# Kernel optimization log

Hardware: AMD Instinct MI355X
Metric: run time of the kernel (lower is better)

Reference implementation:

```python
import jax, jax.numpy as jnp
import numpy as np
from jax import lax

B, T, D = 512, 512, 8   # batch, history_steps, input_size
H = 256                  # hidden_size


def setup_inputs() -> dict:
    key = jax.random.key(0)
    k1, k2, k3, k4, k5 = jax.random.split(key, 5)
    history = jax.random.normal(k1, (B, T, D), dtype=jnp.float32)
    s = 1.0 / np.sqrt(H)  # torch default init scale for RNN cells / Linear
    W_ih = jax.random.uniform(k2, (4 * H, D), minval=-s, maxval=s, dtype=jnp.float32)
    W_hh = jax.random.uniform(k3, (4 * H, H), minval=-s, maxval=s, dtype=jnp.float32)
    W_out = jax.random.uniform(k4, (2, H), minval=-s, maxval=s, dtype=jnp.float32)
    b_out = jax.random.uniform(k5, (2,), minval=-s, maxval=s, dtype=jnp.float32)
    return {"history": history, "W_ih": W_ih, "W_hh": W_hh, "W_out": W_out, "b_out": b_out}


def reference(history, W_ih, W_hh, W_out, b_out):
    # LSTMCell unrolled over time (bias=False), with per-step Linear(H,2) head.
    Bs = history.shape[0]
    h0 = jnp.zeros((Bs, H), dtype=history.dtype)
    c0 = jnp.zeros((Bs, H), dtype=history.dtype)

    def step(carry, x_t):
        h, c = carry
        gates = x_t @ W_ih.T + h @ W_hh.T            # [B, 4H]
        i, f, g, o = jnp.split(gates, 4, axis=-1)
        i = jax.nn.sigmoid(i)
        f = jax.nn.sigmoid(f)
        g = jnp.tanh(g)
        o = jax.nn.sigmoid(o)
        c_new = f * c + i * g
        h_new = o * jnp.tanh(c_new)
        logit = h_new @ W_out.T + b_out              # [B, 2]
        return (h_new, c_new), logit

    x_seq = jnp.transpose(history, (1, 0, 2))        # [T, B, D]
    (h_T, c_T), logits = lax.scan(step, (h0, c0), x_seq)
    logits = jnp.transpose(logits, (1, 0, 2))        # [B, T, 2]
    return logits, h_T, c_T
```

## Files before the change

### kernel.cpp

```cpp
#include <hip/hip_runtime.h>


#define T_STEPS 512
#define B_ROWS  512
#define D_IN    8
#define HID     256

typedef _Float16 half2_t __attribute__((ext_vector_type(2)));

#if defined(__has_builtin)
#  if __has_builtin(__builtin_amdgcn_fdot2)
#    define HAVE_FDOT2 1
#  endif
#endif
#ifndef HAVE_FDOT2
#  define HAVE_FDOT2 0
#endif

#define PW2_ENTRIES (128 * HID)
#define PWIH_FLOATS (4 * HID * D_IN)
#define WS_BYTES_NEEDED ((size_t)PW2_ENTRIES * 16 + (size_t)PWIH_FLOATS * 4)

__global__ void prep_kernel(const float* __restrict__ Wih,
                            const float* __restrict__ Whh,
                            uint4* __restrict__ PW2,
                            float* __restrict__ PWih) {
  int p = blockIdx.x * 256 + threadIdx.x;
  if (p < PW2_ENTRIES) {
    int u = p & (HID - 1), k2 = p >> 8;
    unsigned int g[4];
    #pragma unroll
    for (int gi = 0; gi < 4; ++gi) {
      float lo = Whh[(gi * HID + u) * HID + 2 * k2];
      float hi = Whh[(gi * HID + u) * HID + 2 * k2 + 1];
      half2_t hv;
      hv[0] = (_Float16)lo;
      hv[1] = (_Float16)hi;
      g[gi] = __builtin_bit_cast(unsigned int, hv);
    }
    PW2[p] = make_uint4(g[0], g[1], g[2], g[3]);
  } else {
    int q = p - PW2_ENTRIES;
    if (q < PWIH_FLOATS) {
      int gg = q & 3, u = (q >> 2) & (HID - 1), d = q >> 10;
      PWih[q] = Wih[(gg * HID + u) * D_IN + d];
    }
  }
}

__device__ __forceinline__ float sigmoidf_(float x) {
  return 1.f / (1.f + expf(-x));
}
__device__ __forceinline__ float tanhf_(float x) {
  float e = expf(2.f * x);
  return 1.f - 2.f / (e + 1.f);
}

__device__ __forceinline__ float dot2f(unsigned int wbits, unsigned int hbits, float acc) {
  half2_t w = __builtin_bit_cast(half2_t, wbits);
  half2_t h = __builtin_bit_cast(half2_t, hbits);
#if HAVE_FDOT2
  return __builtin_amdgcn_fdot2(w, h, acc, false);
#else
  acc = fmaf((float)w[0], (float)h[0], acc);
  return fmaf((float)w[1], (float)h[1], acc);
#endif
}

template <bool DIRECT>
__global__ __launch_bounds__(1024, 4)
void lstm_kernel(const float* __restrict__ hist,
                 const float* __restrict__ Wih,
                 const float* __restrict__ Whh,
                 const float* __restrict__ Wout,
                 const float* __restrict__ bout,
                 const uint4* __restrict__ PW2,
                 const float4* __restrict__ PWih,
                 float* __restrict__ out) {
  __shared__ float4   h4[HID];
  __shared__ _Float16 h16[HID / 2][4][2];
  __shared__ float    wo[2 * HID];
  __shared__ float    part[4][4][4][HID];

  const int t = threadIdx.x;
  const int u = t & (HID - 1);
  const int q = t >> 8;

  if (t < 2 * HID) wo[t] = Wout[t];
  if (t < HID) h4[t] = make_float4(0.f, 0.f, 0.f, 0.f);
  ((_Float16*)h16)[t] = (_Float16)0.f;
  float c_reg = 0.f, h_reg = 0.f;
  const float b0 = bout[0], b1 = bout[1];
  __syncthreads();

  const int row0 = blockIdx.x * 4;
  const float4* __restrict__ xp0 = (const float4*)(hist + (long)(row0 + 0) * T_STEPS * D_IN);
  const float4* __restrict__ xp1 = (const float4*)(hist + (long)(row0 + 1) * T_STEPS * D_IN);
  const float4* __restrict__ xp2 = (const float4*)(hist + (long)(row0 + 2) * T_STEPS * D_IN);
  const float4* __restrict__ xp3 = (const float4*)(hist + (long)(row0 + 3) * T_STEPS * D_IN);
  const uint4* __restrict__ pwq = DIRECT ? nullptr : (PW2 + (size_t)(32 * q) * HID + u);
  const uint4* __restrict__ h16q = (const uint4*)h16;

  for (int step = 0; step < T_STEPS; ++step) {
    float ai0 = 0.f, ai1 = 0.f, ai2 = 0.f, ai3 = 0.f;
    float af0 = 0.f, af1 = 0.f, af2 = 0.f, af3 = 0.f;
    float ag0 = 0.f, ag1 = 0.f, ag2 = 0.f, ag3 = 0.f;
    float ao0 = 0.f, ao1 = 0.f, ao2 = 0.f, ao3 = 0.f;

    if (q == 0) {
      float4 a0 = xp0[2 * step], bb0 = xp0[2 * step + 1];
      float4 a1 = xp1[2 * step], bb1 = xp1[2 * step + 1];
      float4 a2 = xp2[2 * step], bb2 = xp2[2 * step + 1];
      float4 a3 = xp3[2 * step], bb3 = xp3[2 * step + 1];
      float x0[D_IN] = {a0.x, a0.y, a0.z, a0.w, bb0.x, bb0.y, bb0.z, bb0.w};
      float x1[D_IN] = {a1.x, a1.y, a1.z, a1.w, bb1.x, bb1.y, bb1.z, bb1.w};
      float x2[D_IN] = {a2.x, a2.y, a2.z, a2.w, bb2.x, bb2.y, bb2.z, bb2.w};
      float x3[D_IN] = {a3.x, a3.y, a3.z, a3.w, bb3.x, bb3.y, bb3.z, bb3.w};
      #pragma unroll
      for (int d = 0; d < D_IN; ++d) {
        float4 w;
        if (DIRECT) {
          w.x = Wih[(0 * HID + u) * D_IN + d];
          w.y = Wih[(1 * HID + u) * D_IN + d];
          w.z = Wih[(2 * HID + u) * D_IN + d];
          w.w = Wih[(3 * HID + u) * D_IN + d];
        } else {
          w = PWih[d * HID + u];
        }
        ai0 = fmaf(w.x, x0[d], ai0); af0 = fmaf(w.y, x0[d], af0);
        ag0 = fmaf(w.z, x0[d], ag0); ao0 = fmaf(w.w, x0[d], ao0);
        ai1 = fmaf(w.x, x1[d], ai1); af1 = fmaf(w.y, x1[d], af1);
        ag1 = fmaf(w.z, x1[d], ag1); ao1 = fmaf(w.w, x1[d], ao1);
        ai2 = fmaf(w.x, x2[d], ai2); af2 = fmaf(w.y, x2[d], af2);
        ag2 = fmaf(w.z, x2[d], ag2); ao2 = fmaf(w.w, x2[d], ao2);
        ai3 = fmaf(w.x, x3[d], ai3); af3 = fmaf(w.y, x3[d], af3);
        ag3 = fmaf(w.z, x3[d], ag3); ao3 = fmaf(w.w, x3[d], ao3);
      }
    }

    if (DIRECT) {
      #pragma unroll 8
      for (int kk = 0; kk < 32; ++kk) {
        int k = 2 * (32 * q + kk);
        float wiA = Whh[(0 * HID + u) * HID + k], wiB = Whh[(0 * HID + u) * HID + k + 1];
        float wfA = Whh[(1 * HID + u) * HID + k], wfB = Whh[(1 * HID + u) * HID + k + 1];
        float wgA = Whh[(2 * HID + u) * HID + k], wgB = Whh[(2 * HID + u) * HID + k + 1];
        float woA = Whh[(3 * HID + u) * HID + k], woB = Whh[(3 * HID + u) * HID + k + 1];
        float4 hA = h4[k];
        float4 hB = h4[k + 1];
        ai0 = fmaf(wiA, hA.x, ai0); ai1 = fmaf(wiA, hA.y, ai1);
        ai2 = fmaf(wiA, hA.z, ai2); ai3 = fmaf(wiA, hA.w, ai3);
        ai0 = fmaf(wiB, hB.x, ai0); ai1 = fmaf(wiB, hB.y, ai1);
        ai2 = fmaf(wiB, hB.z, ai2); ai3 = fmaf(wiB, hB.w, ai3);
        af0 = fmaf(wfA, hA.x, af0); af1 = fmaf(wfA, hA.y, af1);
        af2 = fmaf(wfA, hA.z, af2); af3 = fmaf(wfA, hA.w, af3);
        af0 = fmaf(wfB, hB.x, af0); af1 = fmaf(wfB, hB.y, af1);
        af2 = fmaf(wfB, hB.z, af2); af3 = fmaf(wfB, hB.w, af3);
        ag0 = fmaf(wgA, hA.x, ag0); ag1 = fmaf(wgA, hA.y, ag1);
        ag2 = fmaf(wgA, hA.z, ag2); ag3 = fmaf(wgA, hA.w, ag3);
        ag0 = fmaf(wgB, hB.x, ag0); ag1 = fmaf(wgB, hB.y, ag1);
        ag2 = fmaf(wgB, hB.z, ag2); ag3 = fmaf(wgB, hB.w, ag3);
        ao0 = fmaf(woA, hA.x, ao0); ao1 = fmaf(woA, hA.y, ao1);
        ao2 = fmaf(woA, hA.z, ao2); ao3 = fmaf(woA, hA.w, ao3);
        ao0 = fmaf(woB, hB.x, ao0); ao1 = fmaf(woB, hB.y, ao1);
        ao2 = fmaf(woB, hB.z, ao2); ao3 = fmaf(woB, hB.w, ao3);
      }
    } else {
      #pragma unroll 8
      for (int kk = 0; kk < 32; ++kk) {
        uint4 w  = pwq[(size_t)kk * HID];
        uint4 hp = h16q[32 * q + kk];
        ai0 = dot2f(w.x, hp.x, ai0); ai1 = dot2f(w.x, hp.y, ai1);
        ai2 = dot2f(w.x, hp.z, ai2); ai3 = dot2f(w.x, hp.w, ai3);
        af0 = dot2f(w.y, hp.x, af0); af1 = dot2f(w.y, hp.y, af1);
        af2 = dot2f(w.y, hp.z, af2); af3 = dot2f(w.y, hp.w, af3);
        ag0 = dot2f(w.z, hp.x, ag0); ag1 = dot2f(w.z, hp.y, ag1);
        ag2 = dot2f(w.z, hp.z, ag2); ag3 = dot2f(w.z, hp.w, ag3);
        ao0 = dot2f(w.w, hp.x, ao0); ao1 = dot2f(w.w, hp.y, ao1);
        ao2 = dot2f(w.w, hp.z, ao2); ao3 = dot2f(w.w, hp.w, ao3);
      }
    }

    part[q][0][0][u] = ai0; part[q][0][1][u] = ai1; part[q][0][2][u] = ai2; part[q][0][3][u] = ai3;
    part[q][1][0][u] = af0; part[q][1][1][u] = af1; part[q][1][2][u] = af2; part[q][1][3][u] = af3;
    part[q][2][0][u] = ag0; part[q][2][1][u] = ag1; part[q][2][2][u] = ag2; part[q][2][3][u] = ag3;
    part[q][3][0][u] = ao0; part[q][3][1][u] = ao1; part[q][3][2][u] = ao2; part[q][3][3][u] = ao3;

    __syncthreads();

    {
      float gi = part[0][0][q][u] + part[1][0][q][u] + part[2][0][q][u] + part[3][0][q][u];
      float gf = part[0][1][q][u] + part[1][1][q][u] + part[2][1][q][u] + part[3][1][q][u];
      float gg = part[0][2][q][u] + part[1][2][q][u] + part[2][2][q][u] + part[3][2][q][u];
      float go = part[0][3][q][u] + part[1][3][q][u] + part[2][3][q][u] + part[3][3][q][u];
      float iv = sigmoidf_(gi), fv = sigmoidf_(gf);
      float gv = tanhf_(gg),    ov = sigmoidf_(go);
      c_reg = fmaf(fv, c_reg, iv * gv);
      h_reg = ov * tanhf_(c_reg);
      ((float*)h4)[u * 4 + q] = h_reg;
      h16[u >> 1][q][u & 1] = (_Float16)h_reg;
    }

    __syncthreads();

    {
      const int wv = t >> 6;
      if (wv < 8) {
        const int lane = t & 63;
        const int r  = wv >> 1;
        const int lg = wv & 1;
        float partial = 0.f;
        #pragma unroll
        for (int m = 0; m < 4; ++m) {
          int k = lane + 64 * m;
          float4 hv = h4[k];
          float hval = (r == 0) ? hv.x : (r == 1) ? hv.y : (r == 2) ? hv.z : hv.w;
          partial = fmaf(hval, wo[lg * HID + k], partial);
        }
        #pragma unroll
        for (int off = 32; off > 0; off >>= 1)
          partial += __shfl_down(partial, off, 64);
        if (lane == 0) {
          long row = (long)row0 + r;
          out[(row * T_STEPS + step) * 2 + lg] = partial + (lg ? b1 : b0);
        }
      }
    }
  }

  const long HOFF = (long)B_ROWS * T_STEPS * 2;
  const long COFF = HOFF + (long)B_ROWS * HID;
  const long grow = (long)row0 + q;
  out[HOFF + grow * HID + u] = h_reg;
  out[COFF + grow * HID + u] = c_reg;
}

extern "C" void kernel_launch(void* const* d_in, const int* in_sizes, int n_in,
                              void* d_out, int out_size, void* d_ws, size_t ws_size,
                              hipStream_t stream) {
  const float* hist = (const float*)d_in[0];
  const float* Wih  = (const float*)d_in[1];
  const float* Whh  = (const float*)d_in[2];
  const float* Wout = (const float*)d_in[3];
  const float* bout = (const float*)d_in[4];
  float* out = (float*)d_out;

  if (ws_size >= WS_BYTES_NEEDED) {
    uint4* PW2  = (uint4*)d_ws;
    float* PWih = (float*)((char*)d_ws + (size_t)PW2_ENTRIES * 16);
    prep_kernel<<<160, 256, 0, stream>>>(Wih, Whh, PW2, PWih);
    lstm_kernel<false><<<B_ROWS / 4, 1024, 0, stream>>>(
        hist, Wih, Whh, Wout, bout, PW2, (const float4*)PWih, out);
  } else {
    lstm_kernel<true><<<B_ROWS / 4, 1024, 0, stream>>>(
        hist, Wih, Whh, Wout, bout, nullptr, nullptr, out);
  }
}
```

Before: 3.312 ms.

## Halve batch rows per block and keep half of recurrent weights in registers

Each block now processes 2 batch rows instead of 4, doubling the grid to 256 blocks so all CUs are occupied. Half of each thread's fp16 recurrent weight slice (16 uint4) is preloaded into registers once, and the other half is streamed from global memory each step, cutting per-step weight traffic. The cost is higher register pressure, which may limit occupancy or cause spills, and half the threads now sit idle during the gate nonlinearity phase.

```diff
diff --git a/kernel.cpp b/kernel.cpp
--- a/kernel.cpp
+++ b/kernel.cpp
@@ -77,45 +77,46 @@
                  const uint4* __restrict__ PW2,
                  const float4* __restrict__ PWih,
                  float* __restrict__ out) {
-  __shared__ float4   h4[HID];
-  __shared__ _Float16 h16[HID / 2][4][2];
+  __shared__ float2   h2s[HID];
+  __shared__ _Float16 h16[HID / 2][2][2];
   __shared__ float    wo[2 * HID];
-  __shared__ float    part[4][4][4][HID];
+  __shared__ float    part[4][4][2][HID];
 
   const int t = threadIdx.x;
   const int u = t & (HID - 1);
   const int q = t >> 8;
 
   if (t < 2 * HID) wo[t] = Wout[t];
-  if (t < HID) h4[t] = make_float4(0.f, 0.f, 0.f, 0.f);
-  ((_Float16*)h16)[t] = (_Float16)0.f;
+  if (t < HID) h2s[t] = make_float2(0.f, 0.f);
+  if (t < 2 * HID) ((_Float16*)h16)[t] = (_Float16)0.f;
   float c_reg = 0.f, h_reg = 0.f;
   const float b0 = bout[0], b1 = bout[1];
   __syncthreads();
 
-  const int row0 = blockIdx.x * 4;
+  const int row0 = blockIdx.x * 2;
   const float4* __restrict__ xp0 = (const float4*)(hist + (long)(row0 + 0) * T_STEPS * D_IN);
   const float4* __restrict__ xp1 = (const float4*)(hist + (long)(row0 + 1) * T_STEPS * D_IN);
-  const float4* __restrict__ xp2 = (const float4*)(hist + (long)(row0 + 2) * T_STEPS * D_IN);
-  const float4* __restrict__ xp3 = (const float4*)(hist + (long)(row0 + 3) * T_STEPS * D_IN);
   const uint4* __restrict__ pwq = DIRECT ? nullptr : (PW2 + (size_t)(32 * q) * HID + u);
-  const uint4* __restrict__ h16q = (const uint4*)h16;
+  const uint2* __restrict__ h16q = (const uint2*)h16;
+
+  uint4 wreg[16];
+  if (!DIRECT) {
+    #pragma unroll
+    for (int j = 0; j < 16; ++j) wreg[j] = pwq[(size_t)j * HID];
+  }
+  const uint4* __restrict__ pws = DIRECT ? nullptr : (pwq + (size_t)16 * HID);
 
   for (int step = 0; step < T_STEPS; ++step) {
-    float ai0 = 0.f, ai1 = 0.f, ai2 = 0.f, ai3 = 0.f;
-    float af0 = 0.f, af1 = 0.f, af2 = 0.f, af3 = 0.f;
-    float ag0 = 0.f, ag1 = 0.f, ag2 = 0.f, ag3 = 0.f;
-    float ao0 = 0.f, ao1 = 0.f, ao2 = 0.f, ao3 = 0.f;
+    float ai0 = 0.f, ai1 = 0.f;
+    float af0 = 0.f, af1 = 0.f;
+    float ag0 = 0.f, ag1 = 0.f;
+    float ao0 = 0.f, ao1 = 0.f;
 
     if (q == 0) {
       float4 a0 = xp0[2 * step], bb0 = xp0[2 * step + 1];
       float4 a1 = xp1[2 * step], bb1 = xp1[2 * step + 1];
-      float4 a2 = xp2[2 * step], bb2 = xp2[2 * step + 1];
-      float4 a3 = xp3[2 * step], bb3 = xp3[2 * step + 1];
       float x0[D_IN] = {a0.x, a0.y, a0.z, a0.w, bb0.x, bb0.y, bb0.z, bb0.w};
       float x1[D_IN] = {a1.x, a1.y, a1.z, a1.w, bb1.x, bb1.y, bb1.z, bb1.w};
-      float x2[D_IN] = {a2.x, a2.y, a2.z, a2.w, bb2.x, bb2.y, bb2.z, bb2.w};
-      float x3[D_IN] = {a3.x, a3.y, a3.z, a3.w, bb3.x, bb3.y, bb3.z, bb3.w};
       #pragma unroll
       for (int d = 0; d < D_IN; ++d) {
         float4 w;
@@ -131,10 +132,6 @@
         ag0 = fmaf(w.z, x0[d], ag0); ao0 = fmaf(w.w, x0[d], ao0);
         ai1 = fmaf(w.x, x1[d], ai1); af1 = fmaf(w.y, x1[d], af1);
         ag1 = fmaf(w.z, x1[d], ag1); ao1 = fmaf(w.w, x1[d], ao1);
-        ai2 = fmaf(w.x, x2[d], ai2); af2 = fmaf(w.y, x2[d], af2);
-        ag2 = fmaf(w.z, x2[d], ag2); ao2 = fmaf(w.w, x2[d], ao2);
-        ai3 = fmaf(w.x, x3[d], ai3); af3 = fmaf(w.y, x3[d], af3);
-        ag3 = fmaf(w.z, x3[d], ag3); ao3 = fmaf(w.w, x3[d], ao3);
       }
     }
 
@@ -146,49 +143,42 @@
         float wfA = Whh[(1 * HID + u) * HID + k], wfB = Whh[(1 * HID + u) * HID + k + 1];
         float wgA = Whh[(2 * HID + u) * HID + k], wgB = Whh[(2 * HID + u) * HID + k + 1];
         float woA = Whh[(3 * HID + u) * HID + k], woB = Whh[(3 * HID + u) * HID + k + 1];
-        float4 hA = h4[k];
-        float4 hB = h4[k + 1];
+        float2 hA = h2s[k];
+        float2 hB = h2s[k + 1];
         ai0 = fmaf(wiA, hA.x, ai0); ai1 = fmaf(wiA, hA.y, ai1);
-        ai2 = fmaf(wiA, hA.z, ai2); ai3 = fmaf(wiA, hA.w, ai3);
         ai0 = fmaf(wiB, hB.x, ai0); ai1 = fmaf(wiB, hB.y, ai1);
-        ai2 = fmaf(wiB, hB.z, ai2); ai3 = fmaf(wiB, hB.w, ai3);
         af0 = fmaf(wfA, hA.x, af0); af1 = fmaf(wfA, hA.y, af1);
-        af2 = fmaf(wfA, hA.z, af2); af3 = fmaf(wfA, hA.w, af3);
         af0 = fmaf(wfB, hB.x, af0); af1 = fmaf(wfB, hB.y, af1);
-        af2 = fmaf(wfB, hB.z, af2); af3 = fmaf(wfB, hB.w, af3);
         ag0 = fmaf(wgA, hA.x, ag0); ag1 = fmaf(wgA, hA.y, ag1);
-        ag2 = fmaf(wgA, hA.z, ag2); ag3 = fmaf(wgA, hA.w, ag3);
         ag0 = fmaf(wgB, hB.x, ag0); ag1 = fmaf(wgB, hB.y, ag1);
-        ag2 = fmaf(wgB, hB.z, ag2); ag3 = fmaf(wgB, hB.w, ag3);
         ao0 = fmaf(woA, hA.x, ao0); ao1 = fmaf(woA, hA.y, ao1);
-        ao2 = fmaf(woA, hA.z, ao2); ao3 = fmaf(woA, hA.w, ao3);
         ao0 = fmaf(woB, hB.x, ao0); ao1 = fmaf(woB, hB.y, ao1);
-        ao2 = fmaf(woB, hB.z, ao2); ao3 = fmaf(woB, hB.w, ao3);
       }
     } else {
-      #pragma unroll 8
-      for (int kk = 0; kk < 32; ++kk) {
-        uint4 w  = pwq[(size_t)kk * HID];
-        uint4 hp = h16q[32 * q + kk];
-        ai0 = dot2f(w.x, hp.x, ai0); ai1 = dot2f(w.x, hp.y, ai1);
-        ai2 = dot2f(w.x, hp.z, ai2); ai3 = dot2f(w.x, hp.w, ai3);
-        af0 = dot2f(w.y, hp.x, af0); af1 = dot2f(w.y, hp.y, af1);
-        af2 = dot2f(w.y, hp.z, af2); af3 = dot2f(w.y, hp.w, af3);
-        ag0 = dot2f(w.z, hp.x, ag0); ag1 = dot2f(w.z, hp.y, ag1);
-        ag2 = dot2f(w.z, hp.z, ag2); ag3 = dot2f(w.z, hp.w, ag3);
-        ao0 = dot2f(w.w, hp.x, ao0); ao1 = dot2f(w.w, hp.y, ao1);
-        ao2 = dot2f(w.w, hp.z, ao2); ao3 = dot2f(w.w, hp.w, ao3);
-      }
-    }
-
-    part[q][0][0][u] = ai0; part[q][0][1][u] = ai1; part[q][0][2][u] = ai2; part[q][0][3][u] = ai3;
-    part[q][1][0][u] = af0; part[q][1][1][u] = af1; part[q][1][2][u] = af2; part[q][1][3][u] = af3;
-    part[q][2][0][u] = ag0; part[q][2][1][u] = ag1; part[q][2][2][u] = ag2; part[q][2][3][u] = ag3;
-    part[q][3][0][u] = ao0; part[q][3][1][u] = ao1; part[q][3][2][u] = ao2; part[q][3][3][u] = ao3;
+      #pragma unroll
+      for (int kk = 0; kk < 16; ++kk) {
+        uint4 ws_ = pws[(size_t)kk * HID];
+        uint2 hr  = h16q[32 * q + kk];
+        ai0 = dot2f(wreg[kk].x, hr.x, ai0); ai1 = dot2f(wreg[kk].x, hr.y, ai1);
+        af0 = dot2f(wreg[kk].y, hr.x, af0); af1 = dot2f(wreg[kk].y, hr.y, af1);
+        ag0 = dot2f(wreg[kk].z, hr.x, ag0); ag1 = dot2f(wreg[kk].z, hr.y, ag1);
+        ao0 = dot2f(wreg[kk].w, hr.x, ao0); ao1 = dot2f(wreg[kk].w, hr.y, ao1);
+        uint2 hs = h16q[32 * q + 16 + kk];
+        ai0 = dot2f(ws_.x, hs.x, ai0); ai1 = dot2f(ws_.x, hs.y, ai1);
+        af0 = dot2f(ws_.y, hs.x, af0); af1 = dot2f(ws_.y, hs.y, af1);
+        ag0 = dot2f(ws_.z, hs.x, ag0); ag1 = dot2f(ws_.z, hs.y, ag1);
+        ao0 = dot2f(ws_.w, hs.x, ao0); ao1 = dot2f(ws_.w, hs.y, ao1);
+      }
+    }
+
+    part[q][0][0][u] = ai0; part[q][0][1][u] = ai1;
+    part[q][1][0][u] = af0; part[q][1][1][u] = af1;
+    part[q][2][0][u] = ag0; part[q][2][1][u] = ag1;
+    part[q][3][0][u] = ao0; part[q][3][1][u] = ao1;
 
     __syncthreads();
 
-    {
+    if (q < 2) {
       float gi = part[0][0][q][u] + part[1][0][q][u] + part[2][0][q][u] + part[3][0][q][u];
       float gf = part[0][1][q][u] + part[1][1][q][u] + part[2][1][q][u] + part[3][1][q][u];
       float gg = part[0][2][q][u] + part[1][2][q][u] + part[2][2][q][u] + part[3][2][q][u];
@@ -197,42 +187,42 @@
       float gv = tanhf_(gg),    ov = sigmoidf_(go);
       c_reg = fmaf(fv, c_reg, iv * gv);
       h_reg = ov * tanhf_(c_reg);
-      ((float*)h4)[u * 4 + q] = h_reg;
+      ((float*)h2s)[u * 2 + q] = h_reg;
       h16[u >> 1][q][u & 1] = (_Float16)h_reg;
     }
 
     __syncthreads();
 
-    {
+    if (t < 256) {
       const int wv = t >> 6;
-      if (wv < 8) {
-        const int lane = t & 63;
-        const int r  = wv >> 1;
-        const int lg = wv & 1;
-        float partial = 0.f;
-        #pragma unroll
-        for (int m = 0; m < 4; ++m) {
-          int k = lane + 64 * m;
-          float4 hv = h4[k];
-          float hval = (r == 0) ? hv.x : (r == 1) ? hv.y : (r == 2) ? hv.z : hv.w;
-          partial = fmaf(hval, wo[lg * HID + k], partial);
-        }
-        #pragma unroll
-        for (int off = 32; off > 0; off >>= 1)
-          partial += __shfl_down(partial, off, 64);
-        if (lane == 0) {
-          long row = (long)row0 + r;
-          out[(row * T_STEPS + step) * 2 + lg] = partial + (lg ? b1 : b0);
-        }
-      }
-    }
-  }
-
-  const long HOFF = (long)B_ROWS * T_STEPS * 2;
-  const long COFF = HOFF + (long)B_ROWS * HID;
-  const long grow = (long)row0 + q;
-  out[HOFF + grow * HID + u] = h_reg;
-  out[COFF + grow * HID + u] = c_reg;
+      const int lane = t & 63;
+      const int r  = wv >> 1;
+      const int lg = wv & 1;
+      float partial = 0.f;
+      #pragma unroll
+      for (int m = 0; m < 4; ++m) {
+        int k = lane + 64 * m;
+        float2 hv = h2s[k];
+        float hval = r ? hv.y : hv.x;
+        partial = fmaf(hval, wo[lg * HID + k], partial);
+      }
+      #pragma unroll
+      for (int off = 32; off > 0; off >>= 1)
+        partial += __shfl_down(partial, off, 64);
+      if (lane == 0) {
+        long row = (long)row0 + r;
+        out[(row * T_STEPS + step) * 2 + lg] = partial + (lg ? b1 : b0);
+      }
+    }
+  }
+
+  if (q < 2) {
+    const long HOFF = (long)B_ROWS * T_STEPS * 2;
+    const long COFF = HOFF + (long)B_ROWS * HID;
+    const long grow = (long)row0 + q;
+    out[HOFF + grow * HID + u] = h_reg;
+    out[COFF + grow * HID + u] = c_reg;
+  }
 }
 
 extern "C" void kernel_launch(void* const* d_in, const int* in_sizes, int n_in,
@@ -249,10 +239,10 @@
     uint4* PW2  = (uint4*)d_ws;
     float* PWih = (float*)((char*)d_ws + (size_t)PW2_ENTRIES * 16);
     prep_kernel<<<160, 256, 0, stream>>>(Wih, Whh, PW2, PWih);
-    lstm_kernel<false><<<B_ROWS / 4, 1024, 0, stream>>>(
+    lstm_kernel<false><<<B_ROWS / 2, 1024, 0, stream>>>(
         hist, Wih, Whh, Wout, bout, PW2, (const float4*)PWih, out);
   } else {
-    lstm_kernel<true><<<B_ROWS / 4, 1024, 0, stream>>>(
+    lstm_kernel<true><<<B_ROWS / 2, 1024, 0, stream>>>(
         hist, Wih, Whh, Wout, bout, nullptr, nullptr, out);
   }
 }
```

Result: slower. 4.737 ms (+43.1%).
